# Optimization experiments

Measured on AMD Instinct MI355X. Metric: run time of the kernel, lower is better.

## Reference

```python
import jax, jax.numpy as jnp
import numpy as np

EPS = 1e-5
B, T, D = 4, 2048, 512
H, DK, DV = 4, 64, 128  # num_heads, head_qk_dim, head_v_dim
LR = 32                 # proj_low_rank_dim


def ln(x, g, b):
    m = jnp.mean(x, -1, keepdims=True)
    v = jnp.var(x, -1, keepdims=True)
    return (x - m) * jax.lax.rsqrt(v + EPS) * g + b


def shift(x):  # token shift: zero-pad one step in time
    return jnp.pad(x, ((0, 0), (1, 0), (0, 0)))[:, :-1]


def setup_inputs() -> dict:
    key = jax.random.key(0)
    ks = iter(jax.random.split(key, 40))
    rn = lambda shape, s=0.02: jax.random.normal(next(ks), shape, jnp.float32) * s
    return dict(
        x=jax.random.normal(next(ks), (B, T, D), jnp.float32),
        ln0_g=jnp.ones((D,), jnp.float32), ln0_b=jnp.zeros((D,), jnp.float32),
        ln1_g=jnp.ones((D,), jnp.float32), ln1_b=jnp.zeros((D,), jnp.float32),
        ln2_g=jnp.ones((D,), jnp.float32), ln2_b=jnp.zeros((D,), jnp.float32),
        xp_mu=jax.random.uniform(next(ks), (D,), jnp.float32),
        xp_w1=rn((5 * LR, D)),
        xp_w2=rn((D, 5 * LR)),
        x_bias=rn((5, D)),
        r_w=rn((H * DK, D)),
        w_A=rn((64, D)), w_B=rn((H * DK, 64)), w_b=rn((H * DK,)),
        k_w=rn((H * DK, D)),
        v_w=rn((H * DV, D)),
        g_w=rn((H * DV, D)),
        bonus=rn((H, DK)),
        gn_g=jnp.ones((DV,), jnp.float32), gn_b=jnp.zeros((DV,), jnp.float32),
        o_w=rn((D, H * DV)),
        fk_mu=jax.random.uniform(next(ks), (D,), jnp.float32),
        fk_w=rn((1024, D)),
        fr_mu=jax.random.uniform(next(ks), (D,), jnp.float32),
        fr_w=rn((D, D)),
        fv_w=rn((D, 1024)),
    )


def reference(x, ln0_g, ln0_b, ln1_g, ln1_b, ln2_g, ln2_b, xp_mu, xp_w1, xp_w2,
              x_bias, r_w, w_A, w_B, w_b, k_w, v_w, g_w, bonus, gn_g, gn_b,
              o_w, fk_mu, fk_w, fr_mu, fr_w, fv_w):
    # --- block pre-norm (layer_idx==0) and attn norm ---
    residual = ln(x, ln0_g, ln0_b)
    h = ln(residual, ln1_g, ln1_b)

    # --- RWKV6 time mixing ---
    delta = shift(h) - h
    xx = jnp.tanh(((h + delta * xp_mu) @ xp_w1.T).reshape(B, T, 5, LR))
    mods = jnp.einsum('btnr,hnr->btnh', xx, xp_w2.reshape(D, 5, LR)) + x_bias
    mr, mw, mk, mv, mg = (mods[:, :, i] for i in range(5))

    r = ((h + delta * mr) @ r_w.T).reshape(B, T, H, DK)
    wl = jnp.tanh((h + delta * mw) @ w_A.T) @ w_B.T + w_b  # LoRA decay proj
    dec = jnp.exp(-jnp.exp(wl)).reshape(B, T, H, DK)       # per-channel decay in (0,1)
    k = ((h + delta * mk) @ k_w.T).reshape(B, T, H, DK)
    v = ((h + delta * mv) @ v_w.T).reshape(B, T, H, DV)
    g = (h + delta * mg) @ g_w.T

    def step(S, inp):
        r_t, k_t, v_t, d_t = inp                           # (B,H,DK),(B,H,DK),(B,H,DV),(B,H,DK)
        kv = k_t[..., :, None] * v_t[..., None, :]          # (B,H,DK,DV)
        o_t = jnp.einsum('bhk,bhkv->bhv', r_t, S + bonus[None, :, :, None] * kv)
        S = d_t[..., None] * S + kv
        return S, o_t

    tf = lambda a: jnp.moveaxis(a, 1, 0)  # time-major for scan
    S0 = jnp.zeros((B, H, DK, DV), x.dtype)
    _, o = jax.lax.scan(step, S0, (tf(r), tf(k), tf(v), tf(dec)))
    o = jnp.moveaxis(o, 0, 1)  # (B,T,H,DV)

    # fused per-head LayerNorm + swish gate, then output proj
    gg = g.reshape(B, T, H, DV)
    o = ln(o, gn_g, gn_b) * (gg * jax.nn.sigmoid(gg))
    a = o.reshape(B, T, H * DV) @ o_w.T

    # --- channel mixing FFN with residual ---
    z = a + residual
    h2 = ln(z, ln2_g, ln2_b)
    d2 = shift(h2) - h2
    kk = jnp.square(jax.nn.relu((h2 + d2 * fk_mu) @ fk_w.T))
    rr = jax.nn.sigmoid((h2 + d2 * fr_mu) @ fr_w.T)
    return z + rr * (kk @ fv_w.T)
```

## Files before the change

kernel.cpp:

```cpp
#include <hip/hip_runtime.h>
#include <math.h>

constexpr int Bq = 4, Tq = 2048, Dq = 512, Hq = 4, DKq = 64, DVq = 128, LRq = 32;
constexpr int Mq = Bq * Tq;
constexpr float EPSq = 1e-5f;
constexpr int CL2 = 32, NC2 = Tq / CL2, BH2 = Bq * Hq;

typedef unsigned short u16;
typedef __attribute__((ext_vector_type(8))) short short8v;
typedef __attribute__((ext_vector_type(4))) float f32x4;

__device__ __forceinline__ u16 f2b(float f) {
    unsigned u = __float_as_uint(f);
    u += 0x7fffu + ((u >> 16) & 1);
    return (u16)(u >> 16);
}

__device__ __forceinline__ void gl_lds16(const void* g, void* l) {
    __builtin_amdgcn_global_load_lds(
        (const __attribute__((address_space(1))) unsigned int*)g,
        (__attribute__((address_space(3))) unsigned int*)l, 16, 0, 0);
}

__global__ __launch_bounds__(256)
void k_ln01(const float* __restrict__ x,
            const float* __restrict__ g0, const float* __restrict__ b0,
            const float* __restrict__ g1, const float* __restrict__ b1,
            float* __restrict__ Rout, float* __restrict__ Hout) {
    __shared__ float red[8];
    int row = blockIdx.x, tid = threadIdx.x;
    const float* xr = x + (size_t)row * Dq;
    float v0 = xr[tid], v1 = xr[tid + 256];

    float s = v0 + v1, q = v0 * v0 + v1 * v1;
#pragma unroll
    for (int o = 32; o; o >>= 1) { s += __shfl_down(s, o); q += __shfl_down(q, o); }
    if ((tid & 63) == 0) { red[tid >> 6] = s; red[4 + (tid >> 6)] = q; }
    __syncthreads();
    s = red[0] + red[1] + red[2] + red[3];
    q = red[4] + red[5] + red[6] + red[7];
    float mean = s * (1.f / Dq);
    float inv = rsqrtf(q * (1.f / Dq) - mean * mean + EPSq);
    float r0 = (v0 - mean) * inv * g0[tid] + b0[tid];
    float r1 = (v1 - mean) * inv * g0[tid + 256] + b0[tid + 256];
    Rout[(size_t)row * Dq + tid] = r0;
    Rout[(size_t)row * Dq + tid + 256] = r1;

    s = r0 + r1; q = r0 * r0 + r1 * r1;
#pragma unroll
    for (int o = 32; o; o >>= 1) { s += __shfl_down(s, o); q += __shfl_down(q, o); }
    __syncthreads();
    if ((tid & 63) == 0) { red[tid >> 6] = s; red[4 + (tid >> 6)] = q; }
    __syncthreads();
    s = red[0] + red[1] + red[2] + red[3];
    q = red[4] + red[5] + red[6] + red[7];
    mean = s * (1.f / Dq);
    inv = rsqrtf(q * (1.f / Dq) - mean * mean + EPSq);
    Hout[(size_t)row * Dq + tid] = (r0 - mean) * inv * g1[tid] + b1[tid];
    Hout[(size_t)row * Dq + tid + 256] = (r1 - mean) * inv * g1[tid + 256] + b1[tid + 256];
}

__global__ __launch_bounds__(256)
void k_ln(const float* __restrict__ in, const float* __restrict__ g,
          const float* __restrict__ b, float* __restrict__ out) {
    __shared__ float red[8];
    int row = blockIdx.x, tid = threadIdx.x;
    const float* xr = in + (size_t)row * Dq;
    float v0 = xr[tid], v1 = xr[tid + 256];
    float s = v0 + v1, q = v0 * v0 + v1 * v1;
#pragma unroll
    for (int o = 32; o; o >>= 1) { s += __shfl_down(s, o); q += __shfl_down(q, o); }
    if ((tid & 63) == 0) { red[tid >> 6] = s; red[4 + (tid >> 6)] = q; }
    __syncthreads();
    s = red[0] + red[1] + red[2] + red[3];
    q = red[4] + red[5] + red[6] + red[7];
    float mean = s * (1.f / Dq);
    float inv = rsqrtf(q * (1.f / Dq) - mean * mean + EPSq);
    out[(size_t)row * Dq + tid] = (v0 - mean) * inv * g[tid] + b[tid];
    out[(size_t)row * Dq + tid + 256] = (v1 - mean) * inv * g[tid + 256] + b[tid + 256];
}

__global__ __launch_bounds__(256)
void k_mix1(const float* __restrict__ h, const float* __restrict__ mu,
            u16* __restrict__ out) {
    int row = blockIdx.x, t = row % Tq;
    const float* hr = h + (size_t)row * Dq;
#pragma unroll
    for (int it = 0; it < 2; it++) {
        int d = threadIdx.x + it * 256;
        float hv = hr[d];
        float pv = t ? hr[d - Dq] : 0.f;
        out[(size_t)row * Dq + d] = f2b(hv + (pv - hv) * mu[d]);
    }
}

__global__ __launch_bounds__(256)
void k_mix2(const float* __restrict__ h, const float* __restrict__ muK,
            const float* __restrict__ muR, u16* __restrict__ outK,
            u16* __restrict__ outR) {
    int row = blockIdx.x, t = row % Tq;
    const float* hr = h + (size_t)row * Dq;
#pragma unroll
    for (int it = 0; it < 2; it++) {
        int d = threadIdx.x + it * 256;
        float hv = hr[d];
        float pv = t ? hr[d - Dq] : 0.f;
        float dl = pv - hv;
        outK[(size_t)row * Dq + d] = f2b(hv + dl * muK[d]);
        outR[(size_t)row * Dq + d] = f2b(hv + dl * muR[d]);
    }
}

struct WConv {
    const float* src[11];
    u16* dst[11];
    int n[11];
    int npad[11];
};
__global__ __launch_bounds__(256)
void k_wconv(WConv wc) {
    int w = blockIdx.y;
    const float* s = wc.src[w];
    u16* d = wc.dst[w];
    int n = wc.n[w], np = wc.npad[w];
    for (int i = blockIdx.x * 256 + threadIdx.x; i < np; i += gridDim.x * 256)
        d[i] = (i < n) ? f2b(s[i]) : (u16)0;
}

enum MEpi { ME_NONE, ME_TANH_F32, ME_TANH_B16, ME_DECAY, ME_RESID,
            ME_RELUSQ_B16, ME_SIGMOID, ME_GATED };

template <int EPI>
__global__ __launch_bounds__(256)
void k_mgemm(const u16* __restrict__ A, int lda,
             const u16* __restrict__ W, int ldw,
             void* __restrict__ Cout, int ldc,
             int N, int K,
             const float* __restrict__ bias,
             const float* __restrict__ P1,
             const float* __restrict__ P2) {
    __shared__ __align__(16) char smem[32768];
    char* sA = smem;
    char* sB = smem + 16384;
    const int m0 = blockIdx.x * 128, n0 = blockIdx.y * 128;
    const int tid = threadIdx.x, lane = tid & 63, wid = tid >> 6;
    const int wm = wid >> 1, wn = wid & 1;

    f32x4 acc[4][4] = {};

    const int rl = lane >> 3;
    const int ccs = (lane & 7) ^ rl;
    const u16* ga = A + (size_t)(m0 + wid * 32 + rl) * lda + ccs * 8;
    const u16* gb = W + (size_t)(n0 + wid * 32 + rl) * ldw + ccs * 8;
    char* la = sA + (wid * 32) * 128;
    char* lb = sB + (wid * 32) * 128;

    const int nkt = K >> 6;
    for (int kt = 0; kt < nkt; ++kt) {
        const int k0 = kt << 6;
#pragma unroll
        for (int i = 0; i < 4; ++i) {
            gl_lds16(ga + (size_t)(i * 8) * lda + k0, la + i * 8 * 128);
            gl_lds16(gb + (size_t)(i * 8) * ldw + k0, lb + i * 8 * 128);
        }
        asm volatile("s_waitcnt vmcnt(0)" ::: "memory");
        __syncthreads();
#pragma unroll
        for (int ks = 0; ks < 2; ++ks) {
            short8v af[4], bfr[4];
            const int cc = ks * 4 + (lane >> 4);
#pragma unroll
            for (int i = 0; i < 4; ++i) {
                const int mr = wm * 64 + i * 16 + (lane & 15);
                af[i] = *(const short8v*)(sA + mr * 128 + ((cc ^ (mr & 7)) << 4));
                const int nr = wn * 64 + i * 16 + (lane & 15);
                bfr[i] = *(const short8v*)(sB + nr * 128 + ((cc ^ (nr & 7)) << 4));
            }
#pragma unroll
            for (int i = 0; i < 4; ++i)
#pragma unroll
                for (int j = 0; j < 4; ++j)
                    acc[i][j] = __builtin_amdgcn_mfma_f32_16x16x32_bf16(
                        af[i], bfr[j], acc[i][j], 0, 0, 0);
        }
        __syncthreads();
    }

    float* Cf = (float*)Cout;
    u16* Cb = (u16*)Cout;
#pragma unroll
    for (int i = 0; i < 4; ++i) {
        const int row = m0 + wm * 64 + i * 16 + (lane >> 4) * 4;
#pragma unroll
        for (int j = 0; j < 4; ++j) {
            const int col = n0 + wn * 64 + j * 16 + (lane & 15);
            if (col < N) {
#pragma unroll
                for (int r = 0; r < 4; ++r) {
                    const float v = acc[i][j][r];
                    const size_t idx = (size_t)(row + r) * ldc + col;
                    if constexpr (EPI == ME_NONE)        Cf[idx] = v;
                    else if constexpr (EPI == ME_TANH_F32) Cf[idx] = tanhf(v);
                    else if constexpr (EPI == ME_TANH_B16) Cb[idx] = f2b(tanhf(v));
                    else if constexpr (EPI == ME_DECAY)  Cf[idx] = expf(-expf(v + bias[col]));
                    else if constexpr (EPI == ME_RESID)  Cf[idx] = v + P1[idx];
                    else if constexpr (EPI == ME_RELUSQ_B16) {
                        float t = fmaxf(v, 0.f); Cb[idx] = f2b(t * t);
                    }
                    else if constexpr (EPI == ME_SIGMOID) Cf[idx] = 1.f / (1.f + __expf(-v));
                    else                                  Cf[idx] = P1[idx] + P2[idx] * v;
                }
            }
        }
    }
}

__global__ __launch_bounds__(256)
void k_gemm_mix5(const float* __restrict__ XX, const float* __restrict__ w2,
                 const float* __restrict__ xb, const float* __restrict__ Hb,
                 u16* __restrict__ AMX) {
    constexpr int BM = 64, BK = 16, K = LRq, LDX = 5 * LRq;
    __shared__ __align__(16) float sA[BK][BM + 4];
    __shared__ __align__(16) float sB[BK][BM + 4];
    int g = blockIdx.z;
    const float* A = XX + g * LRq;
    const float* W = w2 + g * LRq;
    const float* bias = xb + g * Dq;
    u16* C = AMX + (size_t)g * Mq * Dq;
    int m0 = blockIdx.x * BM, n0 = blockIdx.y * BM;
    int tid = threadIdx.x;
    int tx = tid & 15, ty = tid >> 4;
    int lr = tid >> 2, lc = (tid & 3) * 4;
    float acc[4][4] = {};

    for (int k0 = 0; k0 < K; k0 += BK) {
        float4 av = *(const float4*)(A + (size_t)(m0 + lr) * LDX + k0 + lc);
        float4 bv = *(const float4*)(W + (size_t)(n0 + lr) * LDX + k0 + lc);
        sA[lc + 0][lr] = av.x; sA[lc + 1][lr] = av.y;
        sA[lc + 2][lr] = av.z; sA[lc + 3][lr] = av.w;
        sB[lc + 0][lr] = bv.x; sB[lc + 1][lr] = bv.y;
        sB[lc + 2][lr] = bv.z; sB[lc + 3][lr] = bv.w;
        __syncthreads();
#pragma unroll
        for (int kk = 0; kk < BK; kk++) {
            float4 a4 = *(const float4*)&sA[kk][ty * 4];
            float4 b4 = *(const float4*)&sB[kk][tx * 4];
            acc[0][0] += a4.x * b4.x; acc[0][1] += a4.x * b4.y;
            acc[0][2] += a4.x * b4.z; acc[0][3] += a4.x * b4.w;
            acc[1][0] += a4.y * b4.x; acc[1][1] += a4.y * b4.y;
            acc[1][2] += a4.y * b4.z; acc[1][3] += a4.y * b4.w;
            acc[2][0] += a4.z * b4.x; acc[2][1] += a4.z * b4.y;
            acc[2][2] += a4.z * b4.z; acc[2][3] += a4.z * b4.w;
            acc[3][0] += a4.w * b4.x; acc[3][1] += a4.w * b4.y;
            acc[3][2] += a4.w * b4.z; acc[3][3] += a4.w * b4.w;
        }
        __syncthreads();
    }

#pragma unroll
    for (int i = 0; i < 4; i++) {
        int row = m0 + ty * 4 + i;
        int t = row % Tq;
#pragma unroll
        for (int j = 0; j < 4; j++) {
            int col = n0 + tx * 4 + j;
            size_t idx = (size_t)row * Dq + col;
            float val = acc[i][j] + bias[col];
            float hv = Hb[idx];
            float pv = t ? Hb[idx - Dq] : 0.f;
            C[idx] = f2b(hv + (pv - hv) * val);
        }
    }
}

__global__ __launch_bounds__(256)
void k_prep_m(const float* __restrict__ Rp, const float* __restrict__ Kp,
              const float* __restrict__ Dp, const float* __restrict__ Vp,
              const float* __restrict__ bonus,
              float* __restrict__ RQd, float* __restrict__ KQg,
              float* __restrict__ DIAG, float* __restrict__ PC,
              float* __restrict__ MC) {
    int c = blockIdx.x, bh = blockIdx.y;
    int b = bh >> 2, h = bh & 3;
    __shared__ float Rl[CL2][68], Kl[CL2][68], Dl[CL2][68];
    __shared__ float Vl[CL2][128];
    __shared__ float Pl[64];
    int tid = threadIdx.x;
#pragma unroll
    for (int i = 0; i < 8; i++) {
        int idx = i * 256 + tid;
        int t = idx >> 6, k = idx & 63;
        size_t g = ((size_t)(b * Tq + c * CL2 + t) * Hq + h) * DKq + k;
        Rl[t][k] = Rp[g]; Kl[t][k] = Kp[g]; Dl[t][k] = Dp[g];
    }
#pragma unroll
    for (int i = 0; i < 16; i++) {
        int idx = i * 256 + tid;
        int t = idx >> 7, v = idx & 127;
        Vl[t][v] = Vp[((size_t)(b * Tq + c * CL2 + t) * Hq + h) * DVq + v];
    }
    __syncthreads();
    {
        int t = tid >> 3, kg = tid & 7;
        float p = 0.f;
#pragma unroll
        for (int i = 0; i < 8; i++) {
            int k = kg * 8 + i;
            p += Rl[t][k] * Kl[t][k] * bonus[h * DKq + k];
        }
        p += __shfl_down(p, 4, 8);
        p += __shfl_down(p, 2, 8);
        p += __shfl_down(p, 1, 8);
        if (kg == 0) DIAG[(size_t)bh * Tq + c * CL2 + t] = p;
    }
    __syncthreads();
    if (tid < 64) {
        int k = tid;
        float p = 1.f;
        for (int t = 0; t < CL2; t++) {
            float d = Dl[t][k];
            Rl[t][k] *= p;
            p *= d;
            Kl[t][k] /= p;
        }
        Pl[k] = p;
    }
    __syncthreads();
#pragma unroll
    for (int i = 0; i < 8; i++) {
        int idx = i * 256 + tid;
        int t = idx >> 6, k = idx & 63;
        size_t g = ((size_t)bh * Tq + c * CL2 + t) * DKq + k;
        RQd[g] = Rl[t][k];
        KQg[g] = Kl[t][k];
    }
    if (tid < 64) PC[(size_t)(bh * NC2 + c) * DKq + tid] = Pl[tid];
    {
        int tk = tid >> 5, tv = tid & 31;
        float acc[8][4] = {};
        for (int t = 0; t < CL2; t++) {
            float4 ka = *(const float4*)&Kl[t][tk * 8];
            float4 kb = *(const float4*)&Kl[t][tk * 8 + 4];
            float4 v4 = *(const float4*)&Vl[t][tv * 4];
            float kv[8] = {ka.x, ka.y, ka.z, ka.w, kb.x, kb.y, kb.z, kb.w};
#pragma unroll
            for (int i = 0; i < 8; i++) {
                acc[i][0] = fmaf(kv[i], v4.x, acc[i][0]);
                acc[i][1] = fmaf(kv[i], v4.y, acc[i][1]);
                acc[i][2] = fmaf(kv[i], v4.z, acc[i][2]);
                acc[i][3] = fmaf(kv[i], v4.w, acc[i][3]);
            }
        }
#pragma unroll
        for (int i = 0; i < 8; i++) {
            int k = tk * 8 + i;
            float P = Pl[k];
            *(float4*)&MC[((size_t)(bh * NC2 + c) * DKq + k) * DVq + tv * 4] =
                make_float4(acc[i][0] * P, acc[i][1] * P, acc[i][2] * P, acc[i][3] * P);
        }
    }
}

__global__ __launch_bounds__(256)
void k_combine2(float* __restrict__ S0MC, const float* __restrict__ PC) {
    int idx = blockIdx.x * 256 + threadIdx.x;
    int v = idx & 127;
    int k = (idx >> 7) & 63;
    int bh = idx >> 13;
    float s = 0.f;
    for (int c = 0; c < NC2; c++) {
        size_t p = (size_t)(bh * NC2 + c) * DKq + k;
        size_t m = p * DVq + v;
        float mc = S0MC[m];
        S0MC[m] = s;
        s = fmaf(PC[p], s, mc);
    }
}

__global__ __launch_bounds__(256)
void k_scan_o(const float* __restrict__ RQd, const float* __restrict__ KQg,
              const float* __restrict__ Vp, const float* __restrict__ S0,
              const float* __restrict__ DIAG, float* __restrict__ O) {
    int c = blockIdx.x, bh = blockIdx.y;
    int b = bh >> 2, h = bh & 3;
    __shared__ float RQl[CL2][68];
    __shared__ float KQt[DKq][36];
    __shared__ float Vl[CL2][128];
    __shared__ float S0l[DKq][128];
    __shared__ float Al[CL2][33];
    int tid = threadIdx.x;
#pragma unroll
    for (int i = 0; i < 8; i++) {
        int idx = i * 256 + tid;
        int t = idx >> 6, k = idx & 63;
        size_t g = ((size_t)bh * Tq + c * CL2 + t) * DKq + k;
        RQl[t][k] = RQd[g];
        KQt[k][t] = KQg[g];
    }
#pragma unroll
    for (int i = 0; i < 16; i++) {
        int idx = i * 256 + tid;
        int t = idx >> 7, v = idx & 127;
        Vl[t][v] = Vp[((size_t)(b * Tq + c * CL2 + t) * Hq + h) * DVq + v];
    }
#pragma unroll
    for (int i = 0; i < 32; i++) {
        int idx = i * 256 + tid;
        int k = idx >> 7, v = idx & 127;
        S0l[k][v] = S0[((size_t)(bh * NC2 + c) * DKq + k) * DVq + v];
    }
    __syncthreads();
    {
        int t = tid >> 3, sq = tid & 7;
        float a[4] = {};
        for (int k = 0; k < DKq; k++) {
            float rq = RQl[t][k];
            float4 k4 = *(const float4*)&KQt[k][sq * 4];
            a[0] = fmaf(rq, k4.x, a[0]);
            a[1] = fmaf(rq, k4.y, a[1]);
            a[2] = fmaf(rq, k4.z, a[2]);
            a[3] = fmaf(rq, k4.w, a[3]);
        }
        float diag = DIAG[(size_t)bh * Tq + c * CL2 + t];
#pragma unroll
        for (int j = 0; j < 4; j++) {
            int s = sq * 4 + j;
            Al[t][s] = (s < t) ? a[j] : (s == t ? diag : 0.f);
        }
    }
    __syncthreads();
    {
        int t = tid >> 3, vg = tid & 7;
        float o[16] = {};
        for (int s = 0; s <= t; s++) {
            float a = Al[t][s];
#pragma unroll
            for (int q = 0; q < 4; q++) {
                float4 v4 = *(const float4*)&Vl[s][vg * 4 + q * 32];
                o[q * 4 + 0] = fmaf(a, v4.x, o[q * 4 + 0]);
                o[q * 4 + 1] = fmaf(a, v4.y, o[q * 4 + 1]);
                o[q * 4 + 2] = fmaf(a, v4.z, o[q * 4 + 2]);
                o[q * 4 + 3] = fmaf(a, v4.w, o[q * 4 + 3]);
            }
        }
        for (int k = 0; k < DKq; k++) {
            float rq = RQl[t][k];
#pragma unroll
            for (int q = 0; q < 4; q++) {
                float4 s4 = *(const float4*)&S0l[k][vg * 4 + q * 32];
                o[q * 4 + 0] = fmaf(rq, s4.x, o[q * 4 + 0]);
                o[q * 4 + 1] = fmaf(rq, s4.y, o[q * 4 + 1]);
                o[q * 4 + 2] = fmaf(rq, s4.z, o[q * 4 + 2]);
                o[q * 4 + 3] = fmaf(rq, s4.w, o[q * 4 + 3]);
            }
        }
        size_t gb = ((size_t)(b * Tq + c * CL2 + t) * Hq + h) * DVq;
#pragma unroll
        for (int q = 0; q < 4; q++)
            *(float4*)&O[gb + vg * 4 + q * 32] =
                make_float4(o[q * 4], o[q * 4 + 1], o[q * 4 + 2], o[q * 4 + 3]);
    }
}

__global__ __launch_bounds__(128)
void k_gatenorm(const float* __restrict__ O, const float* __restrict__ G,
                const float* __restrict__ gn_g, const float* __restrict__ gn_b,
                u16* __restrict__ OB) {
    int r = blockIdx.x;
    size_t base = (size_t)r * DVq;
    int tid = threadIdx.x;
    float v = O[base + tid];
    float s = v, q = v * v;
#pragma unroll
    for (int o = 32; o; o >>= 1) { s += __shfl_down(s, o); q += __shfl_down(q, o); }
    __shared__ float tmp[4];
    int lane = tid & 63, wid = tid >> 6;
    if (lane == 0) { tmp[wid] = s; tmp[wid + 2] = q; }
    __syncthreads();
    s = tmp[0] + tmp[1]; q = tmp[2] + tmp[3];
    float mean = s * (1.f / DVq);
    float inv = rsqrtf(q * (1.f / DVq) - mean * mean + EPSq);
    float ln = (v - mean) * inv * gn_g[tid] + gn_b[tid];
    float g = G[base + tid];
    OB[base + tid] = f2b(ln * (g / (1.f + __expf(-g))));
}

extern "C" void kernel_launch(void* const* d_in, const int* in_sizes, int n_in,
                              void* d_out, int out_size, void* d_ws, size_t ws_size,
                              hipStream_t stream) {
    const float* x     = (const float*)d_in[0];
    const float* ln0_g = (const float*)d_in[1];
    const float* ln0_b = (const float*)d_in[2];
    const float* ln1_g = (const float*)d_in[3];
    const float* ln1_b = (const float*)d_in[4];
    const float* ln2_g = (const float*)d_in[5];
    const float* ln2_b = (const float*)d_in[6];
    const float* xp_mu = (const float*)d_in[7];
    const float* xp_w1 = (const float*)d_in[8];
    const float* xp_w2 = (const float*)d_in[9];
    const float* x_bias= (const float*)d_in[10];
    const float* r_w   = (const float*)d_in[11];
    const float* w_A   = (const float*)d_in[12];
    const float* w_B   = (const float*)d_in[13];
    const float* w_b   = (const float*)d_in[14];
    const float* k_w   = (const float*)d_in[15];
    const float* v_w   = (const float*)d_in[16];
    const float* g_w   = (const float*)d_in[17];
    const float* bonus = (const float*)d_in[18];
    const float* gn_g  = (const float*)d_in[19];
    const float* gn_b  = (const float*)d_in[20];
    const float* o_w   = (const float*)d_in[21];
    const float* fk_mu = (const float*)d_in[22];
    const float* fk_w  = (const float*)d_in[23];
    const float* fr_mu = (const float*)d_in[24];
    const float* fr_w  = (const float*)d_in[25];
    const float* fv_w  = (const float*)d_in[26];
    float* out = (float*)d_out;
    (void)in_sizes; (void)n_in; (void)out_size; (void)ws_size;

    const size_t MD = (size_t)Mq * Dq;
    float* ws = (float*)d_ws;
    size_t off = 0;
    auto af32 = [&](size_t n) { float* p = ws + off; off += n; return p; };

    float* R    = af32(MD);
    float* Hb   = af32(MD);
    float* XX   = af32((size_t)Mq * 160);
    float* Rproj= af32((size_t)Mq * 256);
    float* DEC  = af32((size_t)Mq * 256);
    float* KB   = af32((size_t)Mq * 256);
    float* VB   = af32(MD);
    float* GB   = af32(MD);
    float* PC   = af32((size_t)BH2 * NC2 * DKq);
    float* S0MC = af32((size_t)BH2 * NC2 * DKq * DVq);
    float* DIAG = af32((size_t)BH2 * Tq);

    u16* us = (u16*)(ws + off);
    size_t uo = 0;
    auto au16 = [&](size_t n) { u16* p = us + uo; uo += n; return p; };
    u16* MX0b = au16(MD);
    u16* AMXb = au16(5 * MD);
    u16* TAb  = au16((size_t)Mq * 64);
    u16* OBb  = au16(MD);
    u16* wb_xp1 = au16(256 * 512);
    u16* wb_r   = au16(256 * 512);
    u16* wb_wA  = au16(128 * 512);
    u16* wb_wB  = au16(256 * 64);
    u16* wb_k   = au16(256 * 512);
    u16* wb_v   = au16(512 * 512);
    u16* wb_g   = au16(512 * 512);
    u16* wb_o   = au16(512 * 512);
    u16* wb_fk  = au16(1024 * 512);
    u16* wb_fr  = au16(512 * 512);
    u16* wb_fv  = au16(512 * 1024);

    float* RQd = (float*)MX0b;
    float* KQg = (float*)(AMXb + 4 * MD);
    float* O   = (float*)(AMXb + 2 * MD);
    float* H2  = O;
    float* Z   = GB;
    float* RRb = VB;
    u16* MXKb = AMXb;
    u16* MXRb = AMXb + MD;
    u16* KKb  = AMXb + 2 * MD;

    WConv wc;
    const float* wsrc[11] = {xp_w1, r_w, w_A, w_B, k_w, v_w, g_w, o_w, fk_w, fr_w, fv_w};
    u16* wdst[11] = {wb_xp1, wb_r, wb_wA, wb_wB, wb_k, wb_v, wb_g, wb_o, wb_fk, wb_fr, wb_fv};
    int wn_[11]  = {160*512, 256*512, 64*512, 256*64, 256*512, 512*512, 512*512,
                    512*512, 1024*512, 512*512, 512*1024};
    int wnp[11]  = {256*512, 256*512, 128*512, 256*64, 256*512, 512*512, 512*512,
                    512*512, 1024*512, 512*512, 512*1024};
    for (int i = 0; i < 11; i++) { wc.src[i] = wsrc[i]; wc.dst[i] = wdst[i];
                                   wc.n[i] = wn_[i]; wc.npad[i] = wnp[i]; }
    k_wconv<<<dim3(64, 11), 256, 0, stream>>>(wc);

    k_ln01<<<Mq, 256, 0, stream>>>(x, ln0_g, ln0_b, ln1_g, ln1_b, R, Hb);

    k_mix1<<<Mq, 256, 0, stream>>>(Hb, xp_mu, MX0b);
    k_mgemm<ME_TANH_F32><<<dim3(64, 2), 256, 0, stream>>>(
        MX0b, 512, wb_xp1, 512, XX, 160, 160, 512, nullptr, nullptr, nullptr);

    k_gemm_mix5<<<dim3(128, 8, 5), 256, 0, stream>>>(XX, xp_w2, x_bias, Hb, AMXb);

    k_mgemm<ME_NONE><<<dim3(64, 2), 256, 0, stream>>>(
        AMXb + 0 * MD, 512, wb_r, 512, Rproj, 256, 256, 512, nullptr, nullptr, nullptr);
    k_mgemm<ME_TANH_B16><<<dim3(64, 1), 256, 0, stream>>>(
        AMXb + 1 * MD, 512, wb_wA, 512, TAb, 64, 64, 512, nullptr, nullptr, nullptr);
    k_mgemm<ME_DECAY><<<dim3(64, 2), 256, 0, stream>>>(
        TAb, 64, wb_wB, 64, DEC, 256, 256, 64, w_b, nullptr, nullptr);
    k_mgemm<ME_NONE><<<dim3(64, 2), 256, 0, stream>>>(
        AMXb + 2 * MD, 512, wb_k, 512, KB, 256, 256, 512, nullptr, nullptr, nullptr);
    k_mgemm<ME_NONE><<<dim3(64, 4), 256, 0, stream>>>(
        AMXb + 3 * MD, 512, wb_v, 512, VB, 512, 512, 512, nullptr, nullptr, nullptr);
    k_mgemm<ME_NONE><<<dim3(64, 4), 256, 0, stream>>>(
        AMXb + 4 * MD, 512, wb_g, 512, GB, 512, 512, 512, nullptr, nullptr, nullptr);

    k_prep_m<<<dim3(NC2, BH2), 256, 0, stream>>>(Rproj, KB, DEC, VB, bonus,
                                                 RQd, KQg, DIAG, PC, S0MC);
    k_combine2<<<(BH2 * DKq * DVq) / 256, 256, 0, stream>>>(S0MC, PC);
    k_scan_o<<<dim3(NC2, BH2), 256, 0, stream>>>(RQd, KQg, VB, S0MC, DIAG, O);

    k_gatenorm<<<Mq * Hq, 128, 0, stream>>>(O, GB, gn_g, gn_b, OBb);
    k_mgemm<ME_RESID><<<dim3(64, 4), 256, 0, stream>>>(
        OBb, 512, wb_o, 512, Z, 512, 512, 512, nullptr, R, nullptr);

    k_ln<<<Mq, 256, 0, stream>>>(Z, ln2_g, ln2_b, H2);
    k_mix2<<<Mq, 256, 0, stream>>>(H2, fk_mu, fr_mu, MXKb, MXRb);
    k_mgemm<ME_RELUSQ_B16><<<dim3(64, 8), 256, 0, stream>>>(
        MXKb, 512, wb_fk, 512, KKb, 1024, 1024, 512, nullptr, nullptr, nullptr);
    k_mgemm<ME_SIGMOID><<<dim3(64, 4), 256, 0, stream>>>(
        MXRb, 512, wb_fr, 512, RRb, 512, 512, 512, nullptr, nullptr, nullptr);
    k_mgemm<ME_GATED><<<dim3(64, 4), 256, 0, stream>>>(
        KKb, 1024, wb_fv, 1024, out, 512, 512, 1024, nullptr, Z, RRb);
}
```

Baseline: 468.7 us.

## Batch projection GEMMs into grouped launches and fuse gate-norm and LN2 into neighbors

Five time-mix projection GEMMs and the two FFN input GEMMs are each merged into a single grouped GEMM launch that uses a per-block descriptor table. The per-head group norm and swish gate move into the scan output kernel, so the fp32 O buffer is no longer written and re-read. LN2 is folded into the channel-mix shift kernel by recomputing the previous row's norm, which removes the H2 round trip. In exchange, the grouped GEMM branches on the epilogue at runtime, and each row's LayerNorm statistics are computed twice.

```diff
diff --git a/kernel.cpp b/kernel.cpp
--- a/kernel.cpp
+++ b/kernel.cpp
@@ -61,26 +61,6 @@
 }
 
 __global__ __launch_bounds__(256)
-void k_ln(const float* __restrict__ in, const float* __restrict__ g,
-          const float* __restrict__ b, float* __restrict__ out) {
-    __shared__ float red[8];
-    int row = blockIdx.x, tid = threadIdx.x;
-    const float* xr = in + (size_t)row * Dq;
-    float v0 = xr[tid], v1 = xr[tid + 256];
-    float s = v0 + v1, q = v0 * v0 + v1 * v1;
-#pragma unroll
-    for (int o = 32; o; o >>= 1) { s += __shfl_down(s, o); q += __shfl_down(q, o); }
-    if ((tid & 63) == 0) { red[tid >> 6] = s; red[4 + (tid >> 6)] = q; }
-    __syncthreads();
-    s = red[0] + red[1] + red[2] + red[3];
-    q = red[4] + red[5] + red[6] + red[7];
-    float mean = s * (1.f / Dq);
-    float inv = rsqrtf(q * (1.f / Dq) - mean * mean + EPSq);
-    out[(size_t)row * Dq + tid] = (v0 - mean) * inv * g[tid] + b[tid];
-    out[(size_t)row * Dq + tid + 256] = (v1 - mean) * inv * g[tid + 256] + b[tid + 256];
-}
-
-__global__ __launch_bounds__(256)
 void k_mix1(const float* __restrict__ h, const float* __restrict__ mu,
             u16* __restrict__ out) {
     int row = blockIdx.x, t = row % Tq;
@@ -95,19 +75,43 @@
 }
 
 __global__ __launch_bounds__(256)
-void k_mix2(const float* __restrict__ h, const float* __restrict__ muK,
-            const float* __restrict__ muR, u16* __restrict__ outK,
-            u16* __restrict__ outR) {
-    int row = blockIdx.x, t = row % Tq;
-    const float* hr = h + (size_t)row * Dq;
+void k_ln2mix(const float* __restrict__ Z,
+              const float* __restrict__ g2, const float* __restrict__ b2,
+              const float* __restrict__ muK, const float* __restrict__ muR,
+              u16* __restrict__ outK, u16* __restrict__ outR) {
+    __shared__ float red[16];
+    int row = blockIdx.x, t = row % Tq, tid = threadIdx.x;
+    const float* zr = Z + (size_t)row * Dq;
+    float c0 = zr[tid], c1 = zr[tid + 256];
+    float p0 = 0.f, p1 = 0.f;
+    if (t) { p0 = zr[tid - Dq]; p1 = zr[tid + 256 - Dq]; }
+    float sc = c0 + c1, qc = c0 * c0 + c1 * c1;
+    float sp = p0 + p1, qp = p0 * p0 + p1 * p1;
+#pragma unroll
+    for (int o = 32; o; o >>= 1) {
+        sc += __shfl_down(sc, o); qc += __shfl_down(qc, o);
+        sp += __shfl_down(sp, o); qp += __shfl_down(qp, o);
+    }
+    if ((tid & 63) == 0) {
+        int w = tid >> 6;
+        red[w] = sc; red[4 + w] = qc; red[8 + w] = sp; red[12 + w] = qp;
+    }
+    __syncthreads();
+    sc = red[0] + red[1] + red[2] + red[3];
+    qc = red[4] + red[5] + red[6] + red[7];
+    sp = red[8] + red[9] + red[10] + red[11];
+    qp = red[12] + red[13] + red[14] + red[15];
+    float mc = sc * (1.f / Dq), ic = rsqrtf(qc * (1.f / Dq) - mc * mc + EPSq);
+    float mp = sp * (1.f / Dq), ip = rsqrtf(qp * (1.f / Dq) - mp * mp + EPSq);
 #pragma unroll
     for (int it = 0; it < 2; it++) {
-        int d = threadIdx.x + it * 256;
-        float hv = hr[d];
-        float pv = t ? hr[d - Dq] : 0.f;
-        float dl = pv - hv;
-        outK[(size_t)row * Dq + d] = f2b(hv + dl * muK[d]);
-        outR[(size_t)row * Dq + d] = f2b(hv + dl * muR[d]);
+        int d = tid + it * 256;
+        float cv = it ? c1 : c0, pv = it ? p1 : p0;
+        float hc = (cv - mc) * ic * g2[d] + b2[d];
+        float hp = t ? ((pv - mp) * ip * g2[d] + b2[d]) : 0.f;
+        float dl = hp - hc;
+        outK[(size_t)row * Dq + d] = f2b(hc + dl * muK[d]);
+        outR[(size_t)row * Dq + d] = f2b(hc + dl * muR[d]);
     }
 }
 
@@ -209,6 +213,89 @@
                     }
                     else if constexpr (EPI == ME_SIGMOID) Cf[idx] = 1.f / (1.f + __expf(-v));
                     else                                  Cf[idx] = P1[idx] + P2[idx] * v;
+                }
+            }
+        }
+    }
+}
+
+struct GemmDesc {
+    const u16* A; const u16* W; void* C;
+    int lda, ldw, ldc, N, K, epi;
+};
+struct MultiDesc {
+    GemmDesc g[5];
+    int gid[16];
+    int ntile[16];
+};
+
+__global__ __launch_bounds__(256)
+void k_mgemm_multi(MultiDesc md) {
+    __shared__ __align__(16) char smem[32768];
+    char* sA = smem;
+    char* sB = smem + 16384;
+    const GemmDesc d = md.g[md.gid[blockIdx.y]];
+    const int m0 = blockIdx.x * 128, n0 = md.ntile[blockIdx.y] * 128;
+    const int tid = threadIdx.x, lane = tid & 63, wid = tid >> 6;
+    const int wm = wid >> 1, wn = wid & 1;
+
+    f32x4 acc[4][4] = {};
+
+    const int rl = lane >> 3;
+    const int ccs = (lane & 7) ^ rl;
+    const u16* ga = d.A + (size_t)(m0 + wid * 32 + rl) * d.lda + ccs * 8;
+    const u16* gb = d.W + (size_t)(n0 + wid * 32 + rl) * d.ldw + ccs * 8;
+    char* la = sA + (wid * 32) * 128;
+    char* lb = sB + (wid * 32) * 128;
+
+    const int nkt = d.K >> 6;
+    for (int kt = 0; kt < nkt; ++kt) {
+        const int k0 = kt << 6;
+#pragma unroll
+        for (int i = 0; i < 4; ++i) {
+            gl_lds16(ga + (size_t)(i * 8) * d.lda + k0, la + i * 8 * 128);
+            gl_lds16(gb + (size_t)(i * 8) * d.ldw + k0, lb + i * 8 * 128);
+        }
+        asm volatile("s_waitcnt vmcnt(0)" ::: "memory");
+        __syncthreads();
+#pragma unroll
+        for (int ks = 0; ks < 2; ++ks) {
+            short8v af[4], bfr[4];
+            const int cc = ks * 4 + (lane >> 4);
+#pragma unroll
+            for (int i = 0; i < 4; ++i) {
+                const int mr = wm * 64 + i * 16 + (lane & 15);
+                af[i] = *(const short8v*)(sA + mr * 128 + ((cc ^ (mr & 7)) << 4));
+                const int nr = wn * 64 + i * 16 + (lane & 15);
+                bfr[i] = *(const short8v*)(sB + nr * 128 + ((cc ^ (nr & 7)) << 4));
+            }
+#pragma unroll
+            for (int i = 0; i < 4; ++i)
+#pragma unroll
+                for (int j = 0; j < 4; ++j)
+                    acc[i][j] = __builtin_amdgcn_mfma_f32_16x16x32_bf16(
+                        af[i], bfr[j], acc[i][j], 0, 0, 0);
+        }
+        __syncthreads();
+    }
+
+    float* Cf = (float*)d.C;
+    u16* Cb = (u16*)d.C;
+#pragma unroll
+    for (int i = 0; i < 4; ++i) {
+        const int row = m0 + wm * 64 + i * 16 + (lane >> 4) * 4;
+#pragma unroll
+        for (int j = 0; j < 4; ++j) {
+            const int col = n0 + wn * 64 + j * 16 + (lane & 15);
+            if (col < d.N) {
+#pragma unroll
+                for (int r = 0; r < 4; ++r) {
+                    const float v = acc[i][j][r];
+                    const size_t idx = (size_t)(row + r) * d.ldc + col;
+                    if (d.epi == 0)      Cf[idx] = v;
+                    else if (d.epi == 1) Cb[idx] = f2b(tanhf(v));
+                    else if (d.epi == 2) { float t = fmaxf(v, 0.f); Cb[idx] = f2b(t * t); }
+                    else                 Cf[idx] = 1.f / (1.f + __expf(-v));
                 }
             }
         }
@@ -380,7 +467,9 @@
 __global__ __launch_bounds__(256)
 void k_scan_o(const float* __restrict__ RQd, const float* __restrict__ KQg,
               const float* __restrict__ Vp, const float* __restrict__ S0,
-              const float* __restrict__ DIAG, float* __restrict__ O) {
+              const float* __restrict__ DIAG, const float* __restrict__ Gp,
+              const float* __restrict__ gng, const float* __restrict__ gnb,
+              u16* __restrict__ OB) {
     int c = blockIdx.x, bh = blockIdx.y;
     int b = bh >> 2, h = bh & 3;
     __shared__ float RQl[CL2][68];
@@ -454,35 +543,31 @@
                 o[q * 4 + 3] = fmaf(rq, s4.w, o[q * 4 + 3]);
             }
         }
+        float s = 0.f, q = 0.f;
+#pragma unroll
+        for (int i = 0; i < 16; i++) { s += o[i]; q += o[i] * o[i]; }
+#pragma unroll
+        for (int off = 4; off; off >>= 1) { s += __shfl_xor(s, off); q += __shfl_xor(q, off); }
+        float mean = s * (1.f / DVq);
+        float inv = rsqrtf(q * (1.f / DVq) - mean * mean + EPSq);
         size_t gb = ((size_t)(b * Tq + c * CL2 + t) * Hq + h) * DVq;
 #pragma unroll
-        for (int q = 0; q < 4; q++)
-            *(float4*)&O[gb + vg * 4 + q * 32] =
-                make_float4(o[q * 4], o[q * 4 + 1], o[q * 4 + 2], o[q * 4 + 3]);
-    }
-}
-
-__global__ __launch_bounds__(128)
-void k_gatenorm(const float* __restrict__ O, const float* __restrict__ G,
-                const float* __restrict__ gn_g, const float* __restrict__ gn_b,
-                u16* __restrict__ OB) {
-    int r = blockIdx.x;
-    size_t base = (size_t)r * DVq;
-    int tid = threadIdx.x;
-    float v = O[base + tid];
-    float s = v, q = v * v;
-#pragma unroll
-    for (int o = 32; o; o >>= 1) { s += __shfl_down(s, o); q += __shfl_down(q, o); }
-    __shared__ float tmp[4];
-    int lane = tid & 63, wid = tid >> 6;
-    if (lane == 0) { tmp[wid] = s; tmp[wid + 2] = q; }
-    __syncthreads();
-    s = tmp[0] + tmp[1]; q = tmp[2] + tmp[3];
-    float mean = s * (1.f / DVq);
-    float inv = rsqrtf(q * (1.f / DVq) - mean * mean + EPSq);
-    float ln = (v - mean) * inv * gn_g[tid] + gn_b[tid];
-    float g = G[base + tid];
-    OB[base + tid] = f2b(ln * (g / (1.f + __expf(-g))));
+        for (int qd = 0; qd < 4; qd++) {
+            int v0i = vg * 4 + qd * 32;
+            float4 g4 = *(const float4*)&Gp[gb + v0i];
+            ushort4 ob;
+            float lnv, gv;
+            gv = g4.x; lnv = (o[qd * 4 + 0] - mean) * inv * gng[v0i + 0] + gnb[v0i + 0];
+            ob.x = f2b(lnv * (gv / (1.f + __expf(-gv))));
+            gv = g4.y; lnv = (o[qd * 4 + 1] - mean) * inv * gng[v0i + 1] + gnb[v0i + 1];
+            ob.y = f2b(lnv * (gv / (1.f + __expf(-gv))));
+            gv = g4.z; lnv = (o[qd * 4 + 2] - mean) * inv * gng[v0i + 2] + gnb[v0i + 2];
+            ob.z = f2b(lnv * (gv / (1.f + __expf(-gv))));
+            gv = g4.w; lnv = (o[qd * 4 + 3] - mean) * inv * gng[v0i + 3] + gnb[v0i + 3];
+            ob.w = f2b(lnv * (gv / (1.f + __expf(-gv))));
+            *(ushort4*)&OB[gb + v0i] = ob;
+        }
+    }
 }
 
 extern "C" void kernel_launch(void* const* d_in, const int* in_sizes, int n_in,
@@ -556,8 +641,6 @@
 
     float* RQd = (float*)MX0b;
     float* KQg = (float*)(AMXb + 4 * MD);
-    float* O   = (float*)(AMXb + 2 * MD);
-    float* H2  = O;
     float* Z   = GB;
     float* RRb = VB;
     u16* MXKb = AMXb;
@@ -583,34 +666,40 @@
 
     k_gemm_mix5<<<dim3(128, 8, 5), 256, 0, stream>>>(XX, xp_w2, x_bias, Hb, AMXb);
 
-    k_mgemm<ME_NONE><<<dim3(64, 2), 256, 0, stream>>>(
-        AMXb + 0 * MD, 512, wb_r, 512, Rproj, 256, 256, 512, nullptr, nullptr, nullptr);
-    k_mgemm<ME_TANH_B16><<<dim3(64, 1), 256, 0, stream>>>(
-        AMXb + 1 * MD, 512, wb_wA, 512, TAb, 64, 64, 512, nullptr, nullptr, nullptr);
+    {
+        MultiDesc md;
+        md.g[0] = {AMXb + 0 * MD, wb_r,  (void*)Rproj, 512, 512, 256, 256, 512, 0};
+        md.g[1] = {AMXb + 1 * MD, wb_wA, (void*)TAb,   512, 512,  64,  64, 512, 1};
+        md.g[2] = {AMXb + 2 * MD, wb_k,  (void*)KB,    512, 512, 256, 256, 512, 0};
+        md.g[3] = {AMXb + 3 * MD, wb_v,  (void*)VB,    512, 512, 512, 512, 512, 0};
+        md.g[4] = {AMXb + 4 * MD, wb_g,  (void*)GB,    512, 512, 512, 512, 512, 0};
+        int gid[16]   = {0,0, 1, 2,2, 3,3,3,3, 4,4,4,4, 0,0,0};
+        int ntile[16] = {0,1, 0, 0,1, 0,1,2,3, 0,1,2,3, 0,0,0};
+        for (int i = 0; i < 16; i++) { md.gid[i] = gid[i]; md.ntile[i] = ntile[i]; }
+        k_mgemm_multi<<<dim3(64, 13), 256, 0, stream>>>(md);
+    }
     k_mgemm<ME_DECAY><<<dim3(64, 2), 256, 0, stream>>>(
         TAb, 64, wb_wB, 64, DEC, 256, 256, 64, w_b, nullptr, nullptr);
-    k_mgemm<ME_NONE><<<dim3(64, 2), 256, 0, stream>>>(
-        AMXb + 2 * MD, 512, wb_k, 512, KB, 256, 256, 512, nullptr, nullptr, nullptr);
-    k_mgemm<ME_NONE><<<dim3(64, 4), 256, 0, stream>>>(
-        AMXb + 3 * MD, 512, wb_v, 512, VB, 512, 512, 512, nullptr, nullptr, nullptr);
-    k_mgemm<ME_NONE><<<dim3(64, 4), 256, 0, stream>>>(
-        AMXb + 4 * MD, 512, wb_g, 512, GB, 512, 512, 512, nullptr, nullptr, nullptr);
 
     k_prep_m<<<dim3(NC2, BH2), 256, 0, stream>>>(Rproj, KB, DEC, VB, bonus,
                                                  RQd, KQg, DIAG, PC, S0MC);
     k_combine2<<<(BH2 * DKq * DVq) / 256, 256, 0, stream>>>(S0MC, PC);
-    k_scan_o<<<dim3(NC2, BH2), 256, 0, stream>>>(RQd, KQg, VB, S0MC, DIAG, O);
-
-    k_gatenorm<<<Mq * Hq, 128, 0, stream>>>(O, GB, gn_g, gn_b, OBb);
+    k_scan_o<<<dim3(NC2, BH2), 256, 0, stream>>>(RQd, KQg, VB, S0MC, DIAG,
+                                                 GB, gn_g, gn_b, OBb);
+
     k_mgemm<ME_RESID><<<dim3(64, 4), 256, 0, stream>>>(
         OBb, 512, wb_o, 512, Z, 512, 512, 512, nullptr, R, nullptr);
 
-    k_ln<<<Mq, 256, 0, stream>>>(Z, ln2_g, ln2_b, H2);
-    k_mix2<<<Mq, 256, 0, stream>>>(H2, fk_mu, fr_mu, MXKb, MXRb);
-    k_mgemm<ME_RELUSQ_B16><<<dim3(64, 8), 256, 0, stream>>>(
-        MXKb, 512, wb_fk, 512, KKb, 1024, 1024, 512, nullptr, nullptr, nullptr);
-    k_mgemm<ME_SIGMOID><<<dim3(64, 4), 256, 0, stream>>>(
-        MXRb, 512, wb_fr, 512, RRb, 512, 512, 512, nullptr, nullptr, nullptr);
+    k_ln2mix<<<Mq, 256, 0, stream>>>(Z, ln2_g, ln2_b, fk_mu, fr_mu, MXKb, MXRb);
+    {
+        MultiDesc md;
+        md.g[0] = {MXKb, wb_fk, (void*)KKb, 512, 512, 1024, 1024, 512, 2};
+        md.g[1] = {MXRb, wb_fr, (void*)RRb, 512, 512,  512,  512, 512, 3};
+        int gid[16]   = {0,0,0,0,0,0,0,0, 1,1,1,1, 0,0,0,0};
+        int ntile[16] = {0,1,2,3,4,5,6,7, 0,1,2,3, 0,0,0,0};
+        for (int i = 0; i < 16; i++) { md.gid[i] = gid[i]; md.ntile[i] = ntile[i]; }
+        k_mgemm_multi<<<dim3(64, 12), 256, 0, stream>>>(md);
+    }
     k_mgemm<ME_GATED><<<dim3(64, 4), 256, 0, stream>>>(
         KKb, 1024, wb_fv, 1024, out, 512, 512, 1024, nullptr, Z, RRb);
 }
```

Result: faster. 432.6 us (-7.7%).
